# Kernel tuning notes

Measured on AMD Instinct MI355X. Metric: run time of the kernel, lower is better.

Reference implementation:

```python
import jax, jax.numpy as jnp
import numpy as np

N, E, G = 50000, 800000, 64
IN, HID, H1, H2, OUT = 128, 64, 4, 4, 10
NEG_SLOPE = 0.2


def gat_layer(h, src, dst, W, attn_l, attn_r, bias, n_nodes, n_heads, d):
    # h: [N, F_in] -> feat: [N, H, D]
    feat = (h @ W).reshape(n_nodes, n_heads, d)
    el = jnp.sum(feat * attn_l, axis=-1)          # [N, H]
    er = jnp.sum(feat * attn_r, axis=-1)          # [N, H]
    e = jax.nn.leaky_relu(el[src] + er[dst], NEG_SLOPE)  # [E, H]
    # edge softmax per destination node (numerically stable)
    m = jax.ops.segment_max(e, dst, num_segments=n_nodes)   # [N, H]
    ex = jnp.exp(e - m[dst])                                 # [E, H]
    s = jax.ops.segment_sum(ex, dst, num_segments=n_nodes)   # [N, H]
    alpha = ex / s[dst]                                      # [E, H]
    msg = alpha[:, :, None] * feat[src]                      # [E, H, D]
    out = jax.ops.segment_sum(msg, dst, num_segments=n_nodes)  # [N, H, D]
    return jax.nn.elu(out + bias.reshape(1, n_heads, d))


def setup_inputs() -> dict:
    key = jax.random.key(0)
    ks = jax.random.split(key, 16)
    x = jax.random.normal(ks[0], (N, IN), dtype=jnp.float32)
    src = jax.random.randint(ks[1], (E,), 0, N, dtype=jnp.int32)
    dst = jax.random.randint(ks[2], (E,), 0, N, dtype=jnp.int32)
    graph_ids = jnp.sort(jax.random.randint(ks[3], (N,), 0, G, dtype=jnp.int32))
    sc1 = 1.0 / np.sqrt(IN)
    sc2 = 1.0 / np.sqrt(HID * H1)
    W1 = jax.random.normal(ks[4], (IN, H1 * HID), dtype=jnp.float32) * sc1
    attn_l1 = jax.random.normal(ks[5], (H1, HID), dtype=jnp.float32) * 0.1
    attn_r1 = jax.random.normal(ks[6], (H1, HID), dtype=jnp.float32) * 0.1
    b1 = jnp.zeros((H1 * HID,), dtype=jnp.float32)
    W2 = jax.random.normal(ks[7], (H1 * HID, H2 * HID), dtype=jnp.float32) * sc2
    attn_l2 = jax.random.normal(ks[8], (H2, HID), dtype=jnp.float32) * 0.1
    attn_r2 = jax.random.normal(ks[9], (H2, HID), dtype=jnp.float32) * 0.1
    b2 = jnp.zeros((H2 * HID,), dtype=jnp.float32)
    fcW = jax.random.normal(ks[10], (HID, OUT), dtype=jnp.float32) * (1.0 / np.sqrt(HID))
    fcb = jnp.zeros((OUT,), dtype=jnp.float32)
    return {"x": x, "src": src, "dst": dst, "graph_ids": graph_ids,
            "W1": W1, "attn_l1": attn_l1, "attn_r1": attn_r1, "b1": b1,
            "W2": W2, "attn_l2": attn_l2, "attn_r2": attn_r2, "b2": b2,
            "fcW": fcW, "fcb": fcb}


def reference(x, src, dst, graph_ids, W1, attn_l1, attn_r1, b1,
              W2, attn_l2, attn_r2, b2, fcW, fcb):
    h = gat_layer(x, src, dst, W1, attn_l1, attn_r1, b1, N, H1, HID)
    h = h.reshape(N, H1 * HID)                    # flatten heads (layer 0)
    h = gat_layer(h, src, dst, W2, attn_l2, attn_r2, b2, N, H2, HID)
    h = h.mean(axis=1)                            # mean over heads (layer 1) -> [N, HID]
    pooled = jax.ops.segment_sum(h, graph_ids, num_segments=G)  # SumPooling -> [G, HID]
    return pooled @ fcW + fcb                     # dropout is identity in eval
```

## Files before the change

### kernel.cpp

```cpp
#include <hip/hip_runtime.h>
#include <math.h>

#define NN 50000
#define MPAD 50048
#define NE 800000
#define NG 64
#define FIN 128
#define FH 256
#define HID 64
#define NH 4
#define NOUT 10
#define NEG_SLOPE 0.2f
#define NSB ((NN + 1023) / 1024)

typedef unsigned short u16;
typedef __attribute__((ext_vector_type(8))) short short8;
typedef __attribute__((ext_vector_type(4))) float f32x4;

static __device__ __forceinline__ float leaky(float x){ return x > 0.f ? x : NEG_SLOPE * x; }
static __device__ __forceinline__ float elu1(float x){ return x > 0.f ? x : (__expf(x) - 1.f); }
static __device__ __forceinline__ float b2f(u16 u){
  union { unsigned int i; float f; } v; v.i = ((unsigned)u) << 16; return v.f;
}
static __device__ __forceinline__ u16 f2b(float f){
  union { float f; unsigned int i; } v; v.f = f;
  unsigned r = v.i + 0x7FFFu + ((v.i >> 16) & 1u);
  return (u16)(r >> 16);
}

static __device__ __forceinline__ void gl_lds16(const u16* g, u16* l){
  __builtin_amdgcn_global_load_lds(
      (const __attribute__((address_space(1))) void*)g,
      (__attribute__((address_space(3))) void*)l, 16, 0, 0);
}

__global__ void k_hist(const int* __restrict__ dst, int* __restrict__ cnt,
                       int* __restrict__ rank){
  int i = blockIdx.x * blockDim.x + threadIdx.x;
  if (i < NE) rank[i] = atomicAdd(&cnt[dst[i]], 1);
}

__global__ __launch_bounds__(256) void k_scan1(const int* __restrict__ cnt,
    int* __restrict__ offs, int* __restrict__ bsum)
{
  __shared__ int wsum[4];
  int t = threadIdx.x;
  int lane = t & 63, wv = t >> 6;
  int base = blockIdx.x * 1024 + t * 4;
  int4 v = make_int4(0, 0, 0, 0);
  if (base + 3 < NN) v = *reinterpret_cast<const int4*>(cnt + base);
  else {
    if (base + 0 < NN) v.x = cnt[base + 0];
    if (base + 1 < NN) v.y = cnt[base + 1];
    if (base + 2 < NN) v.z = cnt[base + 2];
  }
  int s = v.x + v.y + v.z + v.w;
  int incl = s;
  #pragma unroll
  for (int d = 1; d < 64; d <<= 1){
    int u = __shfl_up(incl, d);
    if (lane >= d) incl += u;
  }
  if (lane == 63) wsum[wv] = incl;
  __syncthreads();
  int woff = 0;
  #pragma unroll
  for (int i = 0; i < 4; i++) if (i < wv) woff += wsum[i];
  int texcl = woff + incl - s;
  int e0 = texcl, e1 = e0 + v.x, e2 = e1 + v.y, e3 = e2 + v.z;
  if (base + 3 < NN) *reinterpret_cast<int4*>(offs + base) = make_int4(e0, e1, e2, e3);
  else {
    if (base + 0 < NN) offs[base + 0] = e0;
    if (base + 1 < NN) offs[base + 1] = e1;
    if (base + 2 < NN) offs[base + 2] = e2;
  }
  if (t == 255) bsum[blockIdx.x] = woff + incl;
}

__global__ void k_scan2(const int* __restrict__ bsum, int* __restrict__ bpre,
                        int* __restrict__ offs)
{
  int lane = threadIdx.x;
  int s = (lane < NSB) ? bsum[lane] : 0;
  int incl = s;
  #pragma unroll
  for (int d = 1; d < 64; d <<= 1){
    int u = __shfl_up(incl, d);
    if (lane >= d) incl += u;
  }
  if (lane < NSB) bpre[lane] = incl - s;
  if (lane == 0) offs[NN] = NE;
}

__global__ __launch_bounds__(256) void k_scan3(int* __restrict__ offs,
    const int* __restrict__ bpre)
{
  int add = bpre[blockIdx.x];
  if (add == 0) return;
  int base = blockIdx.x * 1024 + threadIdx.x * 4;
  if (base + 3 < NN){
    int4 v = *reinterpret_cast<int4*>(offs + base);
    v.x += add; v.y += add; v.z += add; v.w += add;
    *reinterpret_cast<int4*>(offs + base) = v;
  } else {
    if (base + 0 < NN) offs[base + 0] += add;
    if (base + 1 < NN) offs[base + 1] += add;
    if (base + 2 < NN) offs[base + 2] += add;
  }
}

__global__ void k_scatter(const int* __restrict__ src, const int* __restrict__ dst,
                          const int* __restrict__ offs, const int* __restrict__ rank,
                          int* __restrict__ csrc){
  int i = blockIdx.x * blockDim.x + threadIdx.x;
  if (i < NE){
    int d = dst[i];
    csrc[offs[d] + rank[i]] = src[i];
  }
}

#define F2B_BLKS (NN * FIN / 4 / 256)
#define W1_BLKS  (FIN * FH / 256)
#define W2_BLKS  (FH * FH / 256)
__global__ void k_prep(const float* __restrict__ x, u16* __restrict__ xh,
                       const float* __restrict__ W1, u16* __restrict__ Wtc1,
                       const float* __restrict__ W2, u16* __restrict__ Wtc2)
{
  int b = blockIdx.x;
  if (b < F2B_BLKS){
    int i = (b * 256 + threadIdx.x) * 4;
    float4 v = *reinterpret_cast<const float4*>(x + i);
    ushort4 o; o.x = f2b(v.x); o.y = f2b(v.y); o.z = f2b(v.z); o.w = f2b(v.w);
    *reinterpret_cast<ushort4*>(xh + i) = o;
  } else if (b < F2B_BLKS + W1_BLKS){
    int e = (b - F2B_BLKS) * 256 + threadIdx.x;
    int k = e >> 8, c = e & 255;
    float w = W1[e];
    u16 hi = f2b(w);
    float lo = w - b2f(hi);
    Wtc1[(size_t)c * 2 * FIN + k] = hi;
    Wtc1[(size_t)c * 2 * FIN + FIN + k] = f2b(lo);
  } else {
    int e = (b - F2B_BLKS - W1_BLKS) * 256 + threadIdx.x;
    int k = e >> 8, c = e & 255;
    float w = W2[e];
    u16 hi = f2b(w);
    float lo = w - b2f(hi);
    Wtc2[(size_t)c * 2 * FH + k] = hi;
    Wtc2[(size_t)c * 2 * FH + FH + k] = f2b(lo);
  }
}

template<int K>
__global__ __launch_bounds__(256) void k_gemm_bf(
    const u16* __restrict__ A, const u16* __restrict__ Wtc, u16* __restrict__ C,
    const float* __restrict__ attn_l, const float* __restrict__ attn_r,
    float* __restrict__ el, float* __restrict__ er)
{
  constexpr int K2 = 2 * K;
  __shared__ union {
    struct { u16 a[64 * 32]; u16 b[256 * 32]; } s;
    u16 ct[64 * 256];
  } L;
  int t = threadIdx.x;
  int wv = t >> 6, lane = t & 63;
  int row0 = blockIdx.x * 64;
  int lr = lane & 15, lk = lane >> 4;

  f32x4 acc[4][4];
  #pragma unroll
  for (int m = 0; m < 4; m++)
    #pragma unroll
    for (int n = 0; n < 4; n++) acc[m][n] = (f32x4){0.f, 0.f, 0.f, 0.f};

  const u16* asrc = A + (size_t)(row0 + wv * 16 + (lane >> 2)) * K + (lane & 3) * 8;
  u16* aldst = &L.s.a[wv * 512];
  const u16* bsrc0 = Wtc + (size_t)(wv * 64 + 0 * 16 + (lane >> 2)) * K2 + (lane & 3) * 8;
  const u16* bsrc1 = Wtc + (size_t)(wv * 64 + 1 * 16 + (lane >> 2)) * K2 + (lane & 3) * 8;
  const u16* bsrc2 = Wtc + (size_t)(wv * 64 + 2 * 16 + (lane >> 2)) * K2 + (lane & 3) * 8;
  const u16* bsrc3 = Wtc + (size_t)(wv * 64 + 3 * 16 + (lane >> 2)) * K2 + (lane & 3) * 8;
  u16* bldst0 = &L.s.b[wv * 2048 + 0 * 512];
  u16* bldst1 = &L.s.b[wv * 2048 + 1 * 512];
  u16* bldst2 = &L.s.b[wv * 2048 + 2 * 512];
  u16* bldst3 = &L.s.b[wv * 2048 + 3 * 512];

  for (int k0 = 0; k0 < K2; k0 += 32){
    int acol = k0 & (K - 1);
    gl_lds16(asrc + acol, aldst);
    gl_lds16(bsrc0 + k0, bldst0);
    gl_lds16(bsrc1 + k0, bldst1);
    gl_lds16(bsrc2 + k0, bldst2);
    gl_lds16(bsrc3 + k0, bldst3);
    __syncthreads();
    short8 af[4], bf[4];
    #pragma unroll
    for (int m = 0; m < 4; m++)
      af[m] = *reinterpret_cast<const short8*>(&L.s.a[(m * 16 + lr) * 32 + lk * 8]);
    #pragma unroll
    for (int n = 0; n < 4; n++)
      bf[n] = *reinterpret_cast<const short8*>(&L.s.b[(wv * 64 + n * 16 + lr) * 32 + lk * 8]);
    #pragma unroll
    for (int m = 0; m < 4; m++)
      #pragma unroll
      for (int n = 0; n < 4; n++)
        acc[m][n] = __builtin_amdgcn_mfma_f32_16x16x32_bf16(af[m], bf[n], acc[m][n], 0, 0, 0);
    __syncthreads();
  }

  int rg = lane >> 4;
  #pragma unroll
  for (int m = 0; m < 4; m++)
    #pragma unroll
    for (int n = 0; n < 4; n++)
      #pragma unroll
      for (int r = 0; r < 4; r++)
        L.ct[(m * 16 + rg * 4 + r) * 256 + wv * 64 + n * 16 + lr] = f2b(acc[m][n][r]);
  __syncthreads();
  #pragma unroll
  for (int l = 0; l < 8; l++){
    int idx = t + l * 256;
    int row = idx >> 5, colg = idx & 31;
    short8 v = *reinterpret_cast<const short8*>(&L.ct[row * 256 + colg * 8]);
    *reinterpret_cast<short8*>(C + (size_t)(row0 + row) * 256 + colg * 8) = v;
  }

  {
    int r = lane >> 2, hh = lane & 3;
    const u16* crow = &L.ct[(wv * 16 + r) * 256 + hh * 64];
    float pl = 0.f, pr = 0.f;
    #pragma unroll
    for (int d8 = 0; d8 < 8; d8++){
      short8 cv = *reinterpret_cast<const short8*>(crow + d8 * 8);
      const float* alp = &attn_l[hh * 64 + d8 * 8];
      const float* arp = &attn_r[hh * 64 + d8 * 8];
      #pragma unroll
      for (int q = 0; q < 8; q++){
        float fv = b2f((u16)cv[q]);
        pl = fmaf(fv, alp[q], pl);
        pr = fmaf(fv, arp[q], pr);
      }
    }
    int orow = row0 + wv * 16 + r;
    el[orow * 4 + hh] = pl;
    er[orow * 4 + hh] = pr;
  }
}

template<int LAYER>
__global__ __launch_bounds__(256) void k_agg2(const u16* __restrict__ feat,
    const float* __restrict__ el, const float* __restrict__ er,
    const int* __restrict__ offs, const int* __restrict__ csrc,
    const float* __restrict__ bias, void* __restrict__ outv)
{
  int wv = threadIdx.x >> 6, lane = threadIdx.x & 63;
  int n = blockIdx.x * 4 + wv;
  if (n >= NN) return;
  int e0 = offs[n];
  int deg = offs[n + 1] - e0;
  int hs = lane & 3, slot = lane >> 2;
  int ha = lane >> 4;
  float erh = er[n * 4 + hs];

  float m = -1e30f, srun = 0.f;
  float a0 = 0.f, a1 = 0.f, a2 = 0.f, a3 = 0.f;

  for (int base = 0; base < deg; base += 16){
    int cnt = min(16, deg - base);
    int idx = base + slot;
    int sj = 0; float v = -1e30f;
    if (idx < deg){
      sj = csrc[e0 + idx];
      v = leaky(el[sj * 4 + hs] + erh);
    }
    float cmax = v;
    #pragma unroll
    for (int d = 4; d < 64; d <<= 1) cmax = fmaxf(cmax, __shfl_xor(cmax, d));
    float nm = fmaxf(m, cmax);
    float fac = __expf(m - nm);
    float ex = __expf(v - nm);
    float csum = ex;
    #pragma unroll
    for (int d = 4; d < 64; d <<= 1) csum += __shfl_xor(csum, d);
    srun = srun * fac + csum;
    m = nm;
    float fa = __shfl(fac, ha);
    a0 *= fa; a1 *= fa; a2 *= fa; a3 *= fa;
    #pragma unroll 4
    for (int jj = 0; jj < cnt; jj++){
      float w = __shfl(ex, jj * 4 + ha);
      int sjj = __shfl(sj, jj * 4);
      ushort4 fv = *reinterpret_cast<const ushort4*>(feat + (size_t)sjj * FH + lane * 4);
      a0 = fmaf(w, b2f(fv.x), a0);
      a1 = fmaf(w, b2f(fv.y), a1);
      a2 = fmaf(w, b2f(fv.z), a2);
      a3 = fmaf(w, b2f(fv.w), a3);
    }
  }

  float invh = (deg > 0) ? 1.f / srun : 0.f;
  float inv = __shfl(invh, ha);
  float4 bv = *reinterpret_cast<const float4*>(&bias[lane * 4]);
  a0 = elu1(a0 * inv + bv.x); a1 = elu1(a1 * inv + bv.y);
  a2 = elu1(a2 * inv + bv.z); a3 = elu1(a3 * inv + bv.w);

  if (LAYER == 1){
    u16* out = (u16*)outv;
    ushort4 o; o.x = f2b(a0); o.y = f2b(a1); o.z = f2b(a2); o.w = f2b(a3);
    *reinterpret_cast<ushort4*>(out + (size_t)n * FH + lane * 4) = o;
  } else {
    float* out = (float*)outv;
    a0 += __shfl_xor(a0, 16); a0 += __shfl_xor(a0, 32);
    a1 += __shfl_xor(a1, 16); a1 += __shfl_xor(a1, 32);
    a2 += __shfl_xor(a2, 16); a2 += __shfl_xor(a2, 32);
    a3 += __shfl_xor(a3, 16); a3 += __shfl_xor(a3, 32);
    if (lane < 16){
      float4 o = make_float4(a0 * 0.25f, a1 * 0.25f, a2 * 0.25f, a3 * 0.25f);
      *reinterpret_cast<float4*>(out + (size_t)n * HID + lane * 4) = o;
    }
  }
}

__global__ __launch_bounds__(256) void k_pool(const float* __restrict__ h2,
    const int* __restrict__ gid, float* __restrict__ pooled)
{
  int wv = threadIdx.x >> 6, lane = threadIdx.x & 63;
  int w = blockIdx.x * 4 + wv;
  int base = w * 64;
  if (base >= NN) return;
  int grp = lane >> 4, c4 = (lane & 15) * 4;
  int curg = -1;
  float4 acc = make_float4(0.f, 0.f, 0.f, 0.f);
  #pragma unroll 4
  for (int it = 0; it < 16; it++){
    int row = base + it * 4 + grp;
    if (row >= NN) break;
    int g = gid[row];
    if (g != curg){
      if (curg >= 0){
        atomicAdd(&pooled[curg * HID + c4 + 0], acc.x);
        atomicAdd(&pooled[curg * HID + c4 + 1], acc.y);
        atomicAdd(&pooled[curg * HID + c4 + 2], acc.z);
        atomicAdd(&pooled[curg * HID + c4 + 3], acc.w);
      }
      curg = g; acc = make_float4(0.f, 0.f, 0.f, 0.f);
    }
    float4 v = *reinterpret_cast<const float4*>(&h2[(size_t)row * HID + c4]);
    acc.x += v.x; acc.y += v.y; acc.z += v.z; acc.w += v.w;
  }
  if (curg >= 0){
    atomicAdd(&pooled[curg * HID + c4 + 0], acc.x);
    atomicAdd(&pooled[curg * HID + c4 + 1], acc.y);
    atomicAdd(&pooled[curg * HID + c4 + 2], acc.z);
    atomicAdd(&pooled[curg * HID + c4 + 3], acc.w);
  }
}

__global__ void k_fc(const float* __restrict__ pooled, const float* __restrict__ fcW,
                     const float* __restrict__ fcb, float* __restrict__ out)
{
  int t = threadIdx.x;
  if (t >= NG * NOUT) return;
  int g = t / NOUT, o = t % NOUT;
  float s = fcb[o];
  for (int d = 0; d < HID; d++) s = fmaf(pooled[g * HID + d], fcW[d * NOUT + o], s);
  out[t] = s;
}

static inline size_t align_up(size_t x){ return (x + 255) & ~(size_t)255; }

extern "C" void kernel_launch(void* const* d_in, const int* in_sizes, int n_in,
                              void* d_out, int out_size, void* d_ws, size_t ws_size,
                              hipStream_t stream) {
  const float* x    = (const float*)d_in[0];
  const int*   src  = (const int*)d_in[1];
  const int*   dst  = (const int*)d_in[2];
  const int*   gid  = (const int*)d_in[3];
  const float* W1   = (const float*)d_in[4];
  const float* al1  = (const float*)d_in[5];
  const float* ar1  = (const float*)d_in[6];
  const float* b1   = (const float*)d_in[7];
  const float* W2   = (const float*)d_in[8];
  const float* al2  = (const float*)d_in[9];
  const float* ar2  = (const float*)d_in[10];
  const float* b2   = (const float*)d_in[11];
  const float* fcW  = (const float*)d_in[12];
  const float* fcb  = (const float*)d_in[13];
  float* out = (float*)d_out;

  char* p = (char*)d_ws;
  int* cnt  = (int*)p; p += align_up((size_t)NN * 4);
  int* offs = (int*)p; p += align_up((size_t)(NN + 1) * 4);
  int* bsum = (int*)p; p += align_up((size_t)NSB * 4);
  int* bpre = (int*)p; p += align_up((size_t)NSB * 4);
  int* rank = (int*)p; p += align_up((size_t)NE * 4);
  int* csrc = (int*)p; p += align_up((size_t)NE * 4);
  u16* xh    = (u16*)p; p += align_up((size_t)MPAD * FIN * 2);
  u16* feath = (u16*)p; p += align_up((size_t)MPAD * FH * 2);
  u16* h1h   = (u16*)p; p += align_up((size_t)MPAD * FH * 2);
  float* elb = (float*)p; p += align_up((size_t)MPAD * NH * 4);
  float* erb = (float*)p; p += align_up((size_t)MPAD * NH * 4);
  float* h2  = (float*)p; p += align_up((size_t)NN * HID * 4);
  float* pooled = (float*)p; p += align_up((size_t)NG * HID * 4);
  u16* Wtc1 = (u16*)p; p += align_up((size_t)FIN * FH * 2 * 2);
  u16* Wtc2 = (u16*)p; p += align_up((size_t)FH * FH * 2 * 2);

  hipMemsetAsync(cnt, 0, (size_t)NN * 4, stream);

  const int EB = (NE + 255) / 256;
  const int NB4 = (NN + 3) / 4;
  const int GB = MPAD / 64;

  k_hist<<<EB, 256, 0, stream>>>(dst, cnt, rank);
  k_scan1<<<NSB, 256, 0, stream>>>(cnt, offs, bsum);
  k_scan2<<<1, 64, 0, stream>>>(bsum, bpre, offs);
  k_scan3<<<NSB, 256, 0, stream>>>(offs, bpre);
  k_scatter<<<EB, 256, 0, stream>>>(src, dst, offs, rank, csrc);

  k_prep<<<F2B_BLKS + W1_BLKS + W2_BLKS, 256, 0, stream>>>(x, xh, W1, Wtc1, W2, Wtc2);

  k_gemm_bf<FIN><<<GB, 256, 0, stream>>>(xh, Wtc1, feath, al1, ar1, elb, erb);
  k_agg2<1><<<NB4, 256, 0, stream>>>(feath, elb, erb, offs, csrc, b1, h1h);

  k_gemm_bf<FH><<<GB, 256, 0, stream>>>(h1h, Wtc2, feath, al2, ar2, elb, erb);
  k_agg2<2><<<NB4, 256, 0, stream>>>(feath, elb, erb, offs, csrc, b2, h2);

  hipMemsetAsync(pooled, 0, (size_t)NG * HID * 4, stream);
  k_pool<<<(NN + 255) / 256, 256, 0, stream>>>(h2, gid, pooled);
  k_fc<<<1, 640, 0, stream>>>(pooled, fcW, fcb, out);
}
```

Baseline: 318.9 us.

## Fuse histogram with prep, drop scan3, widen GEMM tile to 128 rows

Folds the histogram, the bf16 conversion, the weight split and the pooled zeroing into one launch. It removes the scan3 kernel and one memset by adding the block prefix at use sites and taking degree from the count array. Separately, the GEMM moves to 512-thread blocks with 128-row tiles so each B tile is shared across twice the rows. The aim is fewer launches and less weight traffic, at the cost of extra index math in the scatter and aggregation kernels and more LDS per block.

```diff
diff --git a/kernel.cpp b/kernel.cpp
--- a/kernel.cpp
+++ b/kernel.cpp
@@ -34,10 +34,48 @@
       (__attribute__((address_space(3))) void*)l, 16, 0, 0);
 }
 
-__global__ void k_hist(const int* __restrict__ dst, int* __restrict__ cnt,
-                       int* __restrict__ rank){
-  int i = blockIdx.x * blockDim.x + threadIdx.x;
-  if (i < NE) rank[i] = atomicAdd(&cnt[dst[i]], 1);
+#define HIST_BLKS ((NE + 255) / 256)
+#define F2B_BLKS (NN * FIN / 4 / 256)
+#define W1_BLKS  (FIN * FH / 256)
+#define W2_BLKS  (FH * FH / 256)
+__global__ void k_histprep(const int* __restrict__ dst, int* __restrict__ cnt,
+                           int* __restrict__ rank,
+                           const float* __restrict__ x, u16* __restrict__ xh,
+                           const float* __restrict__ W1, u16* __restrict__ Wtc1,
+                           const float* __restrict__ W2, u16* __restrict__ Wtc2,
+                           float* __restrict__ pooled)
+{
+  int b = blockIdx.x;
+  if (b < HIST_BLKS){
+    int i = b * 256 + threadIdx.x;
+    if (i < NE) rank[i] = atomicAdd(&cnt[dst[i]], 1);
+  } else if (b < HIST_BLKS + F2B_BLKS){
+    int i = ((b - HIST_BLKS) * 256 + threadIdx.x) * 4;
+    float4 v = *reinterpret_cast<const float4*>(x + i);
+    ushort4 o; o.x = f2b(v.x); o.y = f2b(v.y); o.z = f2b(v.z); o.w = f2b(v.w);
+    *reinterpret_cast<ushort4*>(xh + i) = o;
+  } else if (b < HIST_BLKS + F2B_BLKS + W1_BLKS){
+    int e = (b - HIST_BLKS - F2B_BLKS) * 256 + threadIdx.x;
+    int k = e >> 8, c = e & 255;
+    float w = W1[e];
+    u16 hi = f2b(w);
+    float lo = w - b2f(hi);
+    Wtc1[(size_t)c * 2 * FIN + k] = hi;
+    Wtc1[(size_t)c * 2 * FIN + FIN + k] = f2b(lo);
+  } else if (b < HIST_BLKS + F2B_BLKS + W1_BLKS + W2_BLKS){
+    int e = (b - HIST_BLKS - F2B_BLKS - W1_BLKS) * 256 + threadIdx.x;
+    int k = e >> 8, c = e & 255;
+    float w = W2[e];
+    u16 hi = f2b(w);
+    float lo = w - b2f(hi);
+    Wtc2[(size_t)c * 2 * FH + k] = hi;
+    Wtc2[(size_t)c * 2 * FH + FH + k] = f2b(lo);
+  } else {
+    float4 z = make_float4(0.f, 0.f, 0.f, 0.f);
+    #pragma unroll
+    for (int l = 0; l < 4; l++)
+      *reinterpret_cast<float4*>(pooled + (l * 256 + threadIdx.x) * 4) = z;
+  }
 }
 
 __global__ __launch_bounds__(256) void k_scan1(const int* __restrict__ cnt,
@@ -77,8 +115,7 @@
   if (t == 255) bsum[blockIdx.x] = woff + incl;
 }
 
-__global__ void k_scan2(const int* __restrict__ bsum, int* __restrict__ bpre,
-                        int* __restrict__ offs)
+__global__ void k_scan2(const int* __restrict__ bsum, int* __restrict__ bpre)
 {
   int lane = threadIdx.x;
   int s = (lane < NSB) ? bsum[lane] : 0;
@@ -89,83 +126,34 @@
     if (lane >= d) incl += u;
   }
   if (lane < NSB) bpre[lane] = incl - s;
-  if (lane == 0) offs[NN] = NE;
-}
-
-__global__ __launch_bounds__(256) void k_scan3(int* __restrict__ offs,
-    const int* __restrict__ bpre)
-{
-  int add = bpre[blockIdx.x];
-  if (add == 0) return;
-  int base = blockIdx.x * 1024 + threadIdx.x * 4;
-  if (base + 3 < NN){
-    int4 v = *reinterpret_cast<int4*>(offs + base);
-    v.x += add; v.y += add; v.z += add; v.w += add;
-    *reinterpret_cast<int4*>(offs + base) = v;
-  } else {
-    if (base + 0 < NN) offs[base + 0] += add;
-    if (base + 1 < NN) offs[base + 1] += add;
-    if (base + 2 < NN) offs[base + 2] += add;
-  }
 }
 
 __global__ void k_scatter(const int* __restrict__ src, const int* __restrict__ dst,
-                          const int* __restrict__ offs, const int* __restrict__ rank,
-                          int* __restrict__ csrc){
+                          const int* __restrict__ offs, const int* __restrict__ bpre,
+                          const int* __restrict__ rank, int* __restrict__ csrc){
   int i = blockIdx.x * blockDim.x + threadIdx.x;
   if (i < NE){
     int d = dst[i];
-    csrc[offs[d] + rank[i]] = src[i];
-  }
-}
-
-#define F2B_BLKS (NN * FIN / 4 / 256)
-#define W1_BLKS  (FIN * FH / 256)
-#define W2_BLKS  (FH * FH / 256)
-__global__ void k_prep(const float* __restrict__ x, u16* __restrict__ xh,
-                       const float* __restrict__ W1, u16* __restrict__ Wtc1,
-                       const float* __restrict__ W2, u16* __restrict__ Wtc2)
-{
-  int b = blockIdx.x;
-  if (b < F2B_BLKS){
-    int i = (b * 256 + threadIdx.x) * 4;
-    float4 v = *reinterpret_cast<const float4*>(x + i);
-    ushort4 o; o.x = f2b(v.x); o.y = f2b(v.y); o.z = f2b(v.z); o.w = f2b(v.w);
-    *reinterpret_cast<ushort4*>(xh + i) = o;
-  } else if (b < F2B_BLKS + W1_BLKS){
-    int e = (b - F2B_BLKS) * 256 + threadIdx.x;
-    int k = e >> 8, c = e & 255;
-    float w = W1[e];
-    u16 hi = f2b(w);
-    float lo = w - b2f(hi);
-    Wtc1[(size_t)c * 2 * FIN + k] = hi;
-    Wtc1[(size_t)c * 2 * FIN + FIN + k] = f2b(lo);
-  } else {
-    int e = (b - F2B_BLKS - W1_BLKS) * 256 + threadIdx.x;
-    int k = e >> 8, c = e & 255;
-    float w = W2[e];
-    u16 hi = f2b(w);
-    float lo = w - b2f(hi);
-    Wtc2[(size_t)c * 2 * FH + k] = hi;
-    Wtc2[(size_t)c * 2 * FH + FH + k] = f2b(lo);
+    csrc[offs[d] + bpre[d >> 10] + rank[i]] = src[i];
   }
 }
 
 template<int K>
-__global__ __launch_bounds__(256) void k_gemm_bf(
+__global__ __launch_bounds__(512) void k_gemm_bf(
     const u16* __restrict__ A, const u16* __restrict__ Wtc, u16* __restrict__ C,
     const float* __restrict__ attn_l, const float* __restrict__ attn_r,
     float* __restrict__ el, float* __restrict__ er)
 {
   constexpr int K2 = 2 * K;
   __shared__ union {
-    struct { u16 a[64 * 32]; u16 b[256 * 32]; } s;
-    u16 ct[64 * 256];
+    struct { u16 a[128 * 32]; u16 b[256 * 32]; } s;
+    u16 ct[128 * 256];
   } L;
   int t = threadIdx.x;
   int wv = t >> 6, lane = t & 63;
-  int row0 = blockIdx.x * 64;
+  int row0 = blockIdx.x * 128;
   int lr = lane & 15, lk = lane >> 4;
+  int wm = wv >> 2, wn = wv & 3;
 
   f32x4 acc[4][4];
   #pragma unroll
@@ -175,30 +163,24 @@
 
   const u16* asrc = A + (size_t)(row0 + wv * 16 + (lane >> 2)) * K + (lane & 3) * 8;
   u16* aldst = &L.s.a[wv * 512];
-  const u16* bsrc0 = Wtc + (size_t)(wv * 64 + 0 * 16 + (lane >> 2)) * K2 + (lane & 3) * 8;
-  const u16* bsrc1 = Wtc + (size_t)(wv * 64 + 1 * 16 + (lane >> 2)) * K2 + (lane & 3) * 8;
-  const u16* bsrc2 = Wtc + (size_t)(wv * 64 + 2 * 16 + (lane >> 2)) * K2 + (lane & 3) * 8;
-  const u16* bsrc3 = Wtc + (size_t)(wv * 64 + 3 * 16 + (lane >> 2)) * K2 + (lane & 3) * 8;
-  u16* bldst0 = &L.s.b[wv * 2048 + 0 * 512];
-  u16* bldst1 = &L.s.b[wv * 2048 + 1 * 512];
-  u16* bldst2 = &L.s.b[wv * 2048 + 2 * 512];
-  u16* bldst3 = &L.s.b[wv * 2048 + 3 * 512];
+  const u16* bsrc0 = Wtc + (size_t)(wv * 32 + (lane >> 2)) * K2 + (lane & 3) * 8;
+  const u16* bsrc1 = Wtc + (size_t)(wv * 32 + 16 + (lane >> 2)) * K2 + (lane & 3) * 8;
+  u16* bldst0 = &L.s.b[wv * 1024];
+  u16* bldst1 = &L.s.b[wv * 1024 + 512];
 
   for (int k0 = 0; k0 < K2; k0 += 32){
     int acol = k0 & (K - 1);
     gl_lds16(asrc + acol, aldst);
     gl_lds16(bsrc0 + k0, bldst0);
     gl_lds16(bsrc1 + k0, bldst1);
-    gl_lds16(bsrc2 + k0, bldst2);
-    gl_lds16(bsrc3 + k0, bldst3);
     __syncthreads();
     short8 af[4], bf[4];
     #pragma unroll
     for (int m = 0; m < 4; m++)
-      af[m] = *reinterpret_cast<const short8*>(&L.s.a[(m * 16 + lr) * 32 + lk * 8]);
+      af[m] = *reinterpret_cast<const short8*>(&L.s.a[(wm * 64 + m * 16 + lr) * 32 + lk * 8]);
     #pragma unroll
     for (int n = 0; n < 4; n++)
-      bf[n] = *reinterpret_cast<const short8*>(&L.s.b[(wv * 64 + n * 16 + lr) * 32 + lk * 8]);
+      bf[n] = *reinterpret_cast<const short8*>(&L.s.b[(wn * 64 + n * 16 + lr) * 32 + lk * 8]);
     #pragma unroll
     for (int m = 0; m < 4; m++)
       #pragma unroll
@@ -214,19 +196,19 @@
     for (int n = 0; n < 4; n++)
       #pragma unroll
       for (int r = 0; r < 4; r++)
-        L.ct[(m * 16 + rg * 4 + r) * 256 + wv * 64 + n * 16 + lr] = f2b(acc[m][n][r]);
+        L.ct[(wm * 64 + m * 16 + rg * 4 + r) * 256 + wn * 64 + n * 16 + lr] = f2b(acc[m][n][r]);
   __syncthreads();
   #pragma unroll
   for (int l = 0; l < 8; l++){
-    int idx = t + l * 256;
+    int idx = t + l * 512;
     int row = idx >> 5, colg = idx & 31;
     short8 v = *reinterpret_cast<const short8*>(&L.ct[row * 256 + colg * 8]);
     *reinterpret_cast<short8*>(C + (size_t)(row0 + row) * 256 + colg * 8) = v;
   }
 
   {
-    int r = lane >> 2, hh = lane & 3;
-    const u16* crow = &L.ct[(wv * 16 + r) * 256 + hh * 64];
+    int r = t >> 2, hh = t & 3;
+    const u16* crow = &L.ct[r * 256 + hh * 64];
     float pl = 0.f, pr = 0.f;
     #pragma unroll
     for (int d8 = 0; d8 < 8; d8++){
@@ -240,7 +222,7 @@
         pr = fmaf(fv, arp[q], pr);
       }
     }
-    int orow = row0 + wv * 16 + r;
+    int orow = row0 + r;
     el[orow * 4 + hh] = pl;
     er[orow * 4 + hh] = pr;
   }
@@ -249,14 +231,15 @@
 template<int LAYER>
 __global__ __launch_bounds__(256) void k_agg2(const u16* __restrict__ feat,
     const float* __restrict__ el, const float* __restrict__ er,
-    const int* __restrict__ offs, const int* __restrict__ csrc,
+    const int* __restrict__ offs, const int* __restrict__ bpre,
+    const int* __restrict__ cnt, const int* __restrict__ csrc,
     const float* __restrict__ bias, void* __restrict__ outv)
 {
   int wv = threadIdx.x >> 6, lane = threadIdx.x & 63;
   int n = blockIdx.x * 4 + wv;
   if (n >= NN) return;
-  int e0 = offs[n];
-  int deg = offs[n + 1] - e0;
+  int e0 = offs[n] + bpre[n >> 10];
+  int deg = cnt[n];
   int hs = lane & 3, slot = lane >> 2;
   int ha = lane >> 4;
   float erh = er[n * 4 + hs];
@@ -265,7 +248,7 @@
   float a0 = 0.f, a1 = 0.f, a2 = 0.f, a3 = 0.f;
 
   for (int base = 0; base < deg; base += 16){
-    int cnt = min(16, deg - base);
+    int cntc = min(16, deg - base);
     int idx = base + slot;
     int sj = 0; float v = -1e30f;
     if (idx < deg){
@@ -286,7 +269,7 @@
     float fa = __shfl(fac, ha);
     a0 *= fa; a1 *= fa; a2 *= fa; a3 *= fa;
     #pragma unroll 4
-    for (int jj = 0; jj < cnt; jj++){
+    for (int jj = 0; jj < cntc; jj++){
       float w = __shfl(ex, jj * 4 + ha);
       int sjj = __shfl(sj, jj * 4);
       ushort4 fv = *reinterpret_cast<const ushort4*>(feat + (size_t)sjj * FH + lane * 4);
@@ -389,7 +372,7 @@
 
   char* p = (char*)d_ws;
   int* cnt  = (int*)p; p += align_up((size_t)NN * 4);
-  int* offs = (int*)p; p += align_up((size_t)(NN + 1) * 4);
+  int* offs = (int*)p; p += align_up((size_t)NN * 4);
   int* bsum = (int*)p; p += align_up((size_t)NSB * 4);
   int* bpre = (int*)p; p += align_up((size_t)NSB * 4);
   int* rank = (int*)p; p += align_up((size_t)NE * 4);
@@ -408,23 +391,20 @@
 
   const int EB = (NE + 255) / 256;
   const int NB4 = (NN + 3) / 4;
-  const int GB = MPAD / 64;
-
-  k_hist<<<EB, 256, 0, stream>>>(dst, cnt, rank);
+  const int GB = MPAD / 128;
+  const int HP = HIST_BLKS + F2B_BLKS + W1_BLKS + W2_BLKS + 1;
+
+  k_histprep<<<HP, 256, 0, stream>>>(dst, cnt, rank, x, xh, W1, Wtc1, W2, Wtc2, pooled);
   k_scan1<<<NSB, 256, 0, stream>>>(cnt, offs, bsum);
-  k_scan2<<<1, 64, 0, stream>>>(bsum, bpre, offs);
-  k_scan3<<<NSB, 256, 0, stream>>>(offs, bpre);
-  k_scatter<<<EB, 256, 0, stream>>>(src, dst, offs, rank, csrc);
-
-  k_prep<<<F2B_BLKS + W1_BLKS + W2_BLKS, 256, 0, stream>>>(x, xh, W1, Wtc1, W2, Wtc2);
-
-  k_gemm_bf<FIN><<<GB, 256, 0, stream>>>(xh, Wtc1, feath, al1, ar1, elb, erb);
-  k_agg2<1><<<NB4, 256, 0, stream>>>(feath, elb, erb, offs, csrc, b1, h1h);
-
-  k_gemm_bf<FH><<<GB, 256, 0, stream>>>(h1h, Wtc2, feath, al2, ar2, elb, erb);
-  k_agg2<2><<<NB4, 256, 0, stream>>>(feath, elb, erb, offs, csrc, b2, h2);
-
-  hipMemsetAsync(pooled, 0, (size_t)NG * HID * 4, stream);
+  k_scan2<<<1, 64, 0, stream>>>(bsum, bpre);
+  k_scatter<<<EB, 256, 0, stream>>>(src, dst, offs, bpre, rank, csrc);
+
+  k_gemm_bf<FIN><<<GB, 512, 0, stream>>>(xh, Wtc1, feath, al1, ar1, elb, erb);
+  k_agg2<1><<<NB4, 256, 0, stream>>>(feath, elb, erb, offs, bpre, cnt, csrc, b1, h1h);
+
+  k_gemm_bf<FH><<<GB, 512, 0, stream>>>(h1h, Wtc2, feath, al2, ar2, elb, erb);
+  k_agg2<2><<<NB4, 256, 0, stream>>>(feath, elb, erb, offs, bpre, cnt, csrc, b2, h2);
+
   k_pool<<<(NN + 255) / 256, 256, 0, stream>>>(h2, gid, pooled);
   k_fc<<<1, 640, 0, stream>>>(pooled, fcW, fcb, out);
 }
```

Result: faster. 301.4 us (-5.5%).
